# Kernel optimization log

Measured on AMD Instinct MI355X. Metric: run time of the kernel, lower is better.

The kernel has to match this reference:

```python
import jax, jax.numpy as jnp
import numpy as np

N = 16384      # total nodes (B graphs x 64 squares)
B = 256        # number of graphs
NODES = 64     # nodes per graph (chess board)
E = 131072     # directed edges (avg degree 8)
F_IN = 128
H = 256
GH = 4         # GAT heads
TH = 8         # transformer heads
L_GNN = 8
L_TF = 6
EPS = 1e-5


def layer_norm(x, g, b):
    m = jnp.mean(x, -1, keepdims=True)
    v = jnp.mean((x - m) ** 2, -1, keepdims=True)
    return (x - m) * jax.lax.rsqrt(v + EPS) * g + b


def setup_inputs() -> dict:
    key = jax.random.key(0)
    ks = iter(jax.random.split(key, 80))

    def nrm(shape, s=0.02):
        return jax.random.normal(next(ks), shape, jnp.float32) * s

    x = jax.random.normal(next(ks), (N, F_IN), jnp.float32)
    gid = jax.random.randint(next(ks), (E,), 0, B)
    off = jax.random.randint(next(ks), (2, E), 0, NODES)
    edge_index = gid[None, :] * NODES + off          # edges stay within a graph
    batch = jnp.arange(N, dtype=jnp.int32) // NODES
    piece_types = jax.random.randint(next(ks), (N,), 1, 7)
    return dict(
        x=x, edge_index=edge_index, batch=batch, piece_types=piece_types,
        emb_w=nrm((H, F_IN)), emb_b=nrm((H,)),
        gat_w=nrm((L_GNN, GH * H, H)), gat_as=nrm((L_GNN, GH, H)),
        gat_ad=nrm((L_GNN, GH, H)), gat_b=nrm((L_GNN, H)),
        gnn_g=jnp.ones((L_GNN, H)), gnn_beta=jnp.zeros((L_GNN, H)),
        ln1_g=jnp.ones((L_TF, H)), ln1_b=jnp.zeros((L_TF, H)),
        in_w=nrm((L_TF, 3 * H, H)), in_b=nrm((L_TF, 3 * H)),
        out_w=nrm((L_TF, H, H)), out_b=nrm((L_TF, H)),
        ln2_g=jnp.ones((L_TF, H)), ln2_b=jnp.zeros((L_TF, H)),
        ff1_w=nrm((L_TF, 4 * H, H)), ff1_b=nrm((L_TF, 4 * H)),
        ff2_w=nrm((L_TF, H, 4 * H)), ff2_b=nrm((L_TF, H)),
        pool_w=nrm((H,)), pool_b=nrm((1,)),
        vw1=nrm((H, H)), vb1=nrm((H,)), vw2=nrm((1, H)), vb2=nrm((1,)),
        pw1=nrm((H, H)), pb1=nrm((H,)), pw2=nrm((H, H)), pb2=nrm((H,)),
        uw1=nrm((H // 2, H)), ub1=nrm((H // 2,)), uw2=nrm((1, H // 2)), ub2=nrm((1,)))


def _forward(x, edge_index, batch, emb_w, emb_b, gat_w, gat_as, gat_ad, gat_b,
             gnn_g, gnn_beta, ln1_g, ln1_b, in_w, in_b, out_w, out_b, ln2_g,
             ln2_b, ff1_w, ff1_b, ff2_w, ff2_b, pool_w, pool_b, vw1, vb1, vw2,
             vb2, pw1, pb1, pw2, pb2, uw1, ub1, uw2, ub2):
    loops = jnp.arange(N, dtype=edge_index.dtype)     # GATConv add_self_loops=True
    src = jnp.concatenate([edge_index[0], loops])
    dst = jnp.concatenate([edge_index[1], loops])
    h = x @ emb_w.T + emb_b                           # [N,H] node embedding

    def gnn_layer(h, p):                              # ResidualGNNLayer
        W, a_s, a_d, bias, g, beta = p
        hp = (h @ W.T).reshape(N, GH, H)              # per-head projection
        al_s = jnp.sum(hp * a_s, -1)                  # [N,GH]
        al_d = jnp.sum(hp * a_d, -1)
        e = jax.nn.leaky_relu(al_s[src] + al_d[dst], 0.2)
        m = jax.ops.segment_max(e, dst, num_segments=N)
        ex = jnp.exp(e - m[dst])                      # segment softmax over dst
        den = jax.ops.segment_sum(ex, dst, num_segments=N)
        alpha = ex / den[dst]
        out = jax.ops.segment_sum(hp[src] * alpha[:, :, None], dst, num_segments=N)
        out = out.mean(1) + bias                      # concat=False -> head mean
        out = jax.nn.gelu(layer_norm(out, g, beta), approximate=False)
        return h + out, None                          # project = Identity

    h, _ = jax.lax.scan(gnn_layer, h, (gat_w, gat_as, gat_ad, gat_b, gnn_g, gnn_beta))

    # nn.MultiheadAttention defaults batch_first=False: axis0 (=B graphs) is the
    # sequence axis, axis1 (=64 nodes) is the batch axis — faithful to the source.
    xt = h.reshape(B, NODES, H)
    HD = H // TH

    def tf_layer(t, p):
        g1, b1, iw, ib, ow, ob, g2, b2, w1, fb1, w2, fb2 = p
        tn = layer_norm(t, g1, b1)
        q, k, v = jnp.split(tn @ iw.T + ib, 3, axis=-1)
        q = q.reshape(B, NODES, TH, HD)
        k = k.reshape(B, NODES, TH, HD)
        v = v.reshape(B, NODES, TH, HD)
        att = jnp.einsum('sbhd,tbhd->bhst', q, k) * (1.0 / HD ** 0.5)
        att = jax.nn.softmax(att, -1)
        o = jnp.einsum('bhst,tbhd->sbhd', att, v).reshape(B, NODES, H)
        t = t + (o @ ow.T + ob)
        tn = layer_norm(t, g2, b2)
        ff = jax.nn.gelu(tn @ w1.T + fb1, approximate=False) @ w2.T + fb2
        return t + ff, None

    xt, _ = jax.lax.scan(tf_layer, xt, (ln1_g, ln1_b, in_w, in_b, out_w, out_b,
                                        ln2_g, ln2_b, ff1_w, ff1_b, ff2_w, ff2_b))
    h = xt.reshape(N, H)

    # global attention pooling: softmax over ALL nodes (dim=0, as in the source)
    aw = jax.nn.softmax(h @ pool_w + pool_b[0], axis=0)
    g_rep = jax.ops.segment_sum(h * aw[:, None], batch, num_segments=B)
    value = jnp.tanh(jax.nn.gelu(g_rep @ vw1.T + vb1, approximate=False) @ vw2.T + vb2)[:, 0]
    policy = jax.nn.gelu(h @ pw1.T + pb1, approximate=False) @ pw2.T + pb2
    unc = jax.nn.softplus(jax.nn.gelu(g_rep @ uw1.T + ub1, approximate=False) @ uw2.T + ub2)[:, 0]
    return value, policy, unc


def reference(x, edge_index, batch, piece_types, emb_w, emb_b, gat_w, gat_as,
              gat_ad, gat_b, gnn_g, gnn_beta, ln1_g, ln1_b, in_w, in_b, out_w,
              out_b, ln2_g, ln2_b, ff1_w, ff1_b, ff2_w, ff2_b, pool_w, pool_b,
              vw1, vb1, vw2, vb2, pw1, pb1, pw2, pb2, uw1, ub1, uw2, ub2):
    # piece_types feeds PositionSpecificFeatureExtractor whose output is dead
    # code in the source forward (never used), so it is omitted here.
    return _forward(x, edge_index, batch, emb_w, emb_b, gat_w, gat_as, gat_ad,
                    gat_b, gnn_g, gnn_beta, ln1_g, ln1_b, in_w, in_b, out_w,
                    out_b, ln2_g, ln2_b, ff1_w, ff1_b, ff2_w, ff2_b, pool_w,
                    pool_b, vw1, vb1, vw2, vb2, pw1, pb1, pw2, pb2, uw1, ub1,
                    uw2, ub2)
```

## Files before the change

### kernel.cpp

```cpp
#include <hip/hip_runtime.h>
#include <hip/hip_bf16.h>

typedef __hip_bfloat16 bf16;
typedef __bf16 bf16x8 __attribute__((ext_vector_type(8)));
typedef float  f32x4  __attribute__((ext_vector_type(4)));

#define N_NODES 16384
#define HDIM    256
#define NE      131072
#define NE2     147456

__device__ __forceinline__ float b2f(bf16 v){ return __bfloat162float(v); }
__device__ __forceinline__ bf16  f2b(float v){ return __float2bfloat16(v); }
__device__ __forceinline__ float us2f(unsigned short u){
  union { unsigned int i; float f; } c; c.i = ((unsigned int)u) << 16; return c.f;
}
__device__ __forceinline__ unsigned short f2us(float f){
  bf16 h = __float2bfloat16(f);
  unsigned short u; __builtin_memcpy(&u, &h, 2); return u;
}
__device__ __forceinline__ float gelu_f(float x){
  return 0.5f * x * (1.0f + erff(x * 0.7071067811865476f));
}
__device__ __forceinline__ float wave_sum(float v){
  #pragma unroll
  for (int o = 32; o > 0; o >>= 1) v += __shfl_xor(v, o);
  return v;
}
__device__ __forceinline__ float wave_max(float v){
  #pragma unroll
  for (int o = 32; o > 0; o >>= 1) v = fmaxf(v, __shfl_xor(v, o));
  return v;
}

__device__ __forceinline__ float4 load4(const float* p){ return *(const float4*)p; }
__device__ __forceinline__ float4 load4(const bf16* p){
  ushort4 u = *(const ushort4*)p;
  return make_float4(us2f(u.x), us2f(u.y), us2f(u.z), us2f(u.w));
}
__device__ __forceinline__ void store4(float* p, float4 v){ *(float4*)p = v; }
__device__ __forceinline__ void store4(bf16* p, float4 v){
  ushort4 u = make_ushort4(f2us(v.x), f2us(v.y), f2us(v.z), f2us(v.w));
  *(ushort4*)p = u;
}
__device__ __forceinline__ void storev(float* p, float4 v){ *(float4*)p = v; }
__device__ __forceinline__ void storev(bf16*  p, float4 v){ store4(p, v); }

__device__ __forceinline__ void async_ld16(const bf16* g, unsigned short* l){
  __builtin_amdgcn_global_load_lds(
      (const __attribute__((address_space(1))) void*)g,
      (__attribute__((address_space(3))) void*)l, 16, 0, 0);
}

__global__ void detect_dtype(const unsigned short* __restrict__ x, int n, int* __restrict__ flags){
  int i = blockIdx.x * 256 + threadIdx.x;
  if (i < n) {
    unsigned short u = x[i];
    if ((u & 0x7F80) == 0x7F80) atomicOr(&flags[1], 1);
  }
}
struct ConvArgs {
  const void* src[35];
  unsigned short* dst[35];
  int cumg[36];
  int n[35];
};
__global__ void conv_all4(ConvArgs a, const int* __restrict__ flags){
  int gi = blockIdx.x * 256 + threadIdx.x;
  if (gi >= a.cumg[35]) return;
  int lo = 0, hi = 34;
  while (lo < hi) { int mid = (lo + hi + 1) >> 1; if (gi >= a.cumg[mid]) lo = mid; else hi = mid - 1; }
  int e0 = (gi - a.cumg[lo]) << 2;
  int n = a.n[lo];
  unsigned short* d = a.dst[lo];
  if (flags[1]) {
    const float* s = (const float*)a.src[lo];
    if (e0 + 4 <= n) {
      float4 v = *(const float4*)(s + e0);
      *(ushort4*)(d + e0) = make_ushort4(f2us(v.x), f2us(v.y), f2us(v.z), f2us(v.w));
    } else {
      for (int t = 0; t < n - e0; ++t) d[e0 + t] = f2us(s[e0 + t]);
    }
  } else {
    const unsigned short* s = (const unsigned short*)a.src[lo];
    if (e0 + 4 <= n) *(ushort4*)(d + e0) = *(const ushort4*)(s + e0);
    else for (int t = 0; t < n - e0; ++t) d[e0 + t] = s[e0 + t];
  }
}
__global__ void emit_out(const unsigned short* __restrict__ stage, void* __restrict__ out,
                         int n, const int* __restrict__ flags){
  int i = blockIdx.x * 256 + threadIdx.x;
  if (i >= n) return;
  if (flags[1]) ((float*)out)[i] = us2f(stage[i]);
  else          ((unsigned short*)out)[i] = stage[i];
}
__global__ void write_sentinel(bf16* out, float v){ out[threadIdx.x] = f2b(v); }

#define GF_GELU 1
#define GF_RES  2
#define GF_MIR  4
#define GF_ALS  8

template<typename TO, int FLAGS>
__global__ __launch_bounds__(256) void gemm2(
    const bf16* __restrict__ A, const bf16* __restrict__ W,
    const bf16* __restrict__ bias, const float* __restrict__ res,
    TO* __restrict__ C, bf16* __restrict__ C2, int M, int Nn, int K,
    const bf16* __restrict__ asp, const bf16* __restrict__ adp,
    float* __restrict__ alsp)
{
  __shared__ __align__(16) char ldsraw[36864];
  unsigned short* sA = (unsigned short*)ldsraw;
  unsigned short* sB = sA + 128 * 64;
  const int tid = threadIdx.x;
  const int wave = tid >> 6, lane = tid & 63;
  const int quad = lane >> 4, l16 = lane & 15;
  const int wm = wave & 1, wn = wave >> 1;
  const int row0 = blockIdx.y << 7, col0 = blockIdx.x << 7;
  const int lr = lane >> 3, lc = lane & 7;

  f32x4 acc[4][4] = {};

  for (int kt = 0; kt < K; kt += 64) {
    #pragma unroll
    for (int it = 0; it < 4; ++it) {
      int r0 = (wave << 5) + (it << 3);
      int rr = r0 + lr;
      int gch = lc ^ (rr & 7);
      async_ld16(A + (size_t)(row0 + rr) * K + kt + (gch << 3), sA + (r0 << 6));
      async_ld16(W + (size_t)(col0 + rr) * K + kt + (gch << 3), sB + (r0 << 6));
    }
    __syncthreads();
    #pragma unroll
    for (int kk = 0; kk < 2; ++kk) {
      bf16x8 af[4];
      #pragma unroll
      for (int i = 0; i < 4; ++i) {
        int m = (wm << 6) + (i << 4) + l16;
        af[i] = *(const bf16x8*)&sA[(m << 6) + ((((kk << 2) + quad) ^ (l16 & 7)) << 3)];
      }
      #pragma unroll
      for (int j = 0; j < 4; ++j) {
        int n = (wn << 6) + (j << 4) + l16;
        bf16x8 bfr = *(const bf16x8*)&sB[(n << 6) + ((((kk << 2) + quad) ^ (l16 & 7)) << 3)];
        #pragma unroll
        for (int i = 0; i < 4; ++i)
          acc[i][j] = __builtin_amdgcn_mfma_f32_16x16x32_bf16(af[i], bfr, acc[i][j], 0, 0, 0);
      }
    }
    __syncthreads();
  }

  float* ct = (float*)ldsraw + wave * (64 * 36);
  #pragma unroll
  for (int p = 0; p < 2; ++p) {
    #pragma unroll
    for (int i = 0; i < 4; ++i)
      #pragma unroll
      for (int r = 0; r < 4; ++r) {
        int row = (i << 4) + (quad << 2) + r;
        ct[row * 36 + l16]      = acc[i][(p << 1) + 0][r];
        ct[row * 36 + 16 + l16] = acc[i][(p << 1) + 1][r];
      }
    float4 sS = make_float4(0.f, 0.f, 0.f, 0.f);
    float4 sD = make_float4(0.f, 0.f, 0.f, 0.f);
    #pragma unroll
    for (int it2 = 0; it2 < 8; ++it2) {
      int row = (it2 << 3) + lr;
      int c4 = lc << 2;
      float4 v = *(const float4*)&ct[row * 36 + c4];
      int gcol = col0 + (wn << 6) + (p << 5) + c4;
      size_t gidx = (size_t)(row0 + (wm << 6) + row) * Nn + gcol;
      if (FLAGS & GF_ALS) {
        float asv = b2f(asp[row0 + (wm << 6) + row]);
        float adv = b2f(adp[row0 + (wm << 6) + row]);
        sS.x += asv * v.x; sS.y += asv * v.y; sS.z += asv * v.z; sS.w += asv * v.w;
        sD.x += adv * v.x; sD.y += adv * v.y; sD.z += adv * v.z; sD.w += adv * v.w;
      }
      if (bias) {
        float4 bv = load4(bias + gcol);
        v.x += bv.x; v.y += bv.y; v.z += bv.z; v.w += bv.w;
      }
      if (FLAGS & GF_GELU) {
        v.x = gelu_f(v.x); v.y = gelu_f(v.y); v.z = gelu_f(v.z); v.w = gelu_f(v.w);
      }
      if (FLAGS & GF_RES) {
        float4 rv = *(const float4*)&res[gidx];
        v.x += rv.x; v.y += rv.y; v.z += rv.z; v.w += rv.w;
      }
      storev(C + gidx, v);
      if (FLAGS & GF_MIR) store4(C2 + gidx, v);
    }
    if (FLAGS & GF_ALS) {
      #pragma unroll
      for (int o = 8; o < 64; o <<= 1) {
        sS.x += __shfl_xor(sS.x, o); sS.y += __shfl_xor(sS.y, o);
        sS.z += __shfl_xor(sS.z, o); sS.w += __shfl_xor(sS.w, o);
        sD.x += __shfl_xor(sD.x, o); sD.y += __shfl_xor(sD.y, o);
        sD.z += __shfl_xor(sD.z, o); sD.w += __shfl_xor(sD.w, o);
      }
      if (lr == 0) {
        int node = col0 + (wn << 6) + (p << 5) + (lc << 2);
        int hd2 = blockIdx.y >> 1;
        int slice = ((blockIdx.y & 1) << 1) | wm;
        *(float4*)&alsp[(size_t)((slice << 3) + hd2) * Nn + node] = sS;
        *(float4*)&alsp[(size_t)((slice << 3) + 4 + hd2) * Nn + node] = sD;
      }
    }
  }
}

__global__ __launch_bounds__(256) void gemm_rln(
    const bf16* __restrict__ A, const bf16* __restrict__ W,
    const bf16* __restrict__ bias, float* __restrict__ h,
    bf16* __restrict__ tn, const bf16* __restrict__ lng,
    const bf16* __restrict__ lnb, int K)
{
  __shared__ __align__(16) char ldsraw[66560];
  unsigned short* sA = (unsigned short*)ldsraw;
  unsigned short* sB = sA + 64 * 64;
  const int tid = threadIdx.x;
  const int wave = tid >> 6, lane = tid & 63;
  const int quad = lane >> 4, l16 = lane & 15;
  const int row0 = blockIdx.x << 6;
  const int lr = lane >> 3, lc = lane & 7;

  f32x4 acc[4][4] = {};

  for (int kt = 0; kt < K; kt += 64) {
    #pragma unroll
    for (int it = 0; it < 2; ++it) {
      int r0 = (wave << 4) + (it << 3);
      int rr = r0 + lr;
      int gch = lc ^ (rr & 7);
      async_ld16(A + (size_t)(row0 + rr) * K + kt + (gch << 3), sA + (r0 << 6));
    }
    #pragma unroll
    for (int it = 0; it < 8; ++it) {
      int r0 = (wave << 6) + (it << 3);
      int rr = r0 + lr;
      int gch = lc ^ (rr & 7);
      async_ld16(W + (size_t)rr * K + kt + (gch << 3), sB + (r0 << 6));
    }
    __syncthreads();
    #pragma unroll
    for (int kk = 0; kk < 2; ++kk) {
      bf16x8 af[4];
      #pragma unroll
      for (int i = 0; i < 4; ++i) {
        int m = (i << 4) + l16;
        af[i] = *(const bf16x8*)&sA[(m << 6) + ((((kk << 2) + quad) ^ (l16 & 7)) << 3)];
      }
      #pragma unroll
      for (int j = 0; j < 4; ++j) {
        int n = (wave << 6) + (j << 4) + l16;
        bf16x8 bfr = *(const bf16x8*)&sB[(n << 6) + ((((kk << 2) + quad) ^ (l16 & 7)) << 3)];
        #pragma unroll
        for (int i = 0; i < 4; ++i)
          acc[i][j] = __builtin_amdgcn_mfma_f32_16x16x32_bf16(af[i], bfr, acc[i][j], 0, 0, 0);
      }
    }
    __syncthreads();
  }

  float* ct = (float*)ldsraw;
  #pragma unroll
  for (int j = 0; j < 4; ++j) {
    int col = (wave << 6) + (j << 4) + l16;
    #pragma unroll
    for (int i = 0; i < 4; ++i)
      #pragma unroll
      for (int r = 0; r < 4; ++r)
        ct[((i << 4) + (quad << 2) + r) * 260 + col] = acc[i][j][r];
  }
  __syncthreads();

  const int row = tid >> 2, q = tid & 3;
  const int c0 = q << 6;
  size_t gr = (size_t)(row0 + row) * 256 + c0;
  float4 v[16];
  float s1 = 0.f;
  #pragma unroll
  for (int k = 0; k < 16; ++k) {
    float4 cv = *(const float4*)&ct[row * 260 + c0 + (k << 2)];
    float4 bv = load4(bias + c0 + (k << 2));
    float4 rv = *(const float4*)&h[gr + (k << 2)];
    v[k].x = cv.x + bv.x + rv.x;
    v[k].y = cv.y + bv.y + rv.y;
    v[k].z = cv.z + bv.z + rv.z;
    v[k].w = cv.w + bv.w + rv.w;
    *(float4*)&h[gr + (k << 2)] = v[k];
    s1 += v[k].x + v[k].y + v[k].z + v[k].w;
  }
  s1 += __shfl_xor(s1, 1); s1 += __shfl_xor(s1, 2);
  float mean = s1 * (1.0f / 256.0f);
  float s2 = 0.f;
  #pragma unroll
  for (int k = 0; k < 16; ++k) {
    float dx = v[k].x - mean, dy = v[k].y - mean, dz = v[k].z - mean, dw = v[k].w - mean;
    s2 += dx * dx + dy * dy + dz * dz + dw * dw;
  }
  s2 += __shfl_xor(s2, 1); s2 += __shfl_xor(s2, 2);
  float rstd = rsqrtf(s2 * (1.0f / 256.0f) + 1e-5f);
  #pragma unroll
  for (int k = 0; k < 16; ++k) {
    float4 gv = load4(lng + c0 + (k << 2));
    float4 bv2 = load4(lnb + c0 + (k << 2));
    float4 y;
    y.x = (v[k].x - mean) * rstd * gv.x + bv2.x;
    y.y = (v[k].y - mean) * rstd * gv.y + bv2.y;
    y.z = (v[k].z - mean) * rstd * gv.z + bv2.z;
    y.w = (v[k].w - mean) * rstd * gv.w + bv2.w;
    store4(tn + gr + (k << 2), y);
  }
}

__global__ void csr_count(const int* __restrict__ edst, int* __restrict__ cnt){
  int e = blockIdx.x * 256 + threadIdx.x;
  if (e < NE2) {
    int d = (e < NE) ? edst[e] : (e - NE);
    atomicAdd(&cnt[d], 1);
  }
}
__global__ __launch_bounds__(1024) void csr_scan(const int* __restrict__ cnt, int* __restrict__ off){
  __shared__ int ls[1024];
  int t = threadIdx.x;
  int base = t * 16;
  int loc[16]; int s = 0;
  #pragma unroll
  for (int j = 0; j < 16; ++j) { loc[j] = s; s += cnt[base + j]; }
  ls[t] = s;
  __syncthreads();
  for (int o = 1; o < 1024; o <<= 1) {
    int v = (t >= o) ? ls[t - o] : 0;
    __syncthreads();
    ls[t] += v;
    __syncthreads();
  }
  int pre = (t == 0) ? 0 : ls[t - 1];
  #pragma unroll
  for (int j = 0; j < 16; ++j) off[base + j] = pre + loc[j];
  if (t == 1023) off[N_NODES] = ls[1023];
}
__global__ void csr_fill(const int* __restrict__ edst, const int* __restrict__ off,
                         int* __restrict__ fillc, int* __restrict__ list){
  int e = blockIdx.x * 256 + threadIdx.x;
  if (e < NE2) {
    int d = (e < NE) ? edst[e] : (e - NE);
    int p = atomicAdd(&fillc[d], 1);
    list[off[d] + p] = e;
  }
}

#define ALF_S 68

__device__ __forceinline__ bf16x8 pack8(const float* v, float scale){
  unsigned short u[8];
  #pragma unroll
  for (int t = 0; t < 8; ++t) u[t] = f2us(v[t] * scale);
  bf16x8 r; __builtin_memcpy(&r, u, 16); return r;
}

__global__ __launch_bounds__(256) void gat_graph2(
    const int* __restrict__ esrc, const bf16* __restrict__ hpT_g,
    const int* __restrict__ off, const int* __restrict__ list,
    const float* __restrict__ alsp,
    bf16* __restrict__ msg4, int g0, int hn)
{
  __shared__ unsigned short hpT[256 * 64];
  __shared__ float alpha[64 * ALF_S];
  __shared__ float als[64], ald[64], dinv[64];

  const int hd = blockIdx.x & 3;
  const int lg = blockIdx.x >> 2;
  const int g  = g0 + lg;
  const int tid = threadIdx.x;
  const int wave = tid >> 6, lane = tid & 63;
  const int quad = lane >> 4, l16 = lane & 15;
  const int nd = tid >> 2;
  const int k4 = tid & 3;

  {
    const int rl = lane >> 3, jj = lane & 7;
    #pragma unroll
    for (int it = 0; it < 8; ++it) {
      int c = (it << 5) + (wave << 3) + rl;
      async_ld16(hpT_g + (size_t)((hd << 8) + c) * 16384 + (g << 6) + ((jj ^ (c & 7)) << 3),
                 hpT + (((it << 5) + (wave << 3)) << 6));
    }
  }
  if (tid < 128) {
    int n2 = tid & 63;
    int sd = (tid >> 6) << 2;
    float v = 0.f;
    #pragma unroll
    for (int sl = 0; sl < 4; ++sl)
      v += alsp[(size_t)((sl << 3) + sd + hd) * 16384 + (g << 6) + n2];
    if (sd) ald[n2] = v; else als[n2] = v;
  }
  #pragma unroll
  for (int idx = tid; idx < 64 * ALF_S; idx += 256) alpha[idx] = 0.f;
  __syncthreads();

  {
    int st = off[(g << 6) + nd];
    int deg = off[(g << 6) + nd + 1] - st;
    float ad = ald[nd];
    float mx = -1e30f;
    for (int e = k4; e < deg; e += 4) {
      int ed = list[st + e];
      int sl = ((ed < NE) ? esrc[ed] : (ed - NE)) - (g << 6);
      float v = als[sl] + ad;
      v = (v > 0.f) ? v : 0.2f * v;
      mx = fmaxf(mx, v);
    }
    mx = fmaxf(mx, __shfl_xor(mx, 1)); mx = fmaxf(mx, __shfl_xor(mx, 2));
    float den = 0.f;
    for (int e = k4; e < deg; e += 4) {
      int ed = list[st + e];
      int sl = ((ed < NE) ? esrc[ed] : (ed - NE)) - (g << 6);
      float v = als[sl] + ad;
      v = (v > 0.f) ? v : 0.2f * v;
      float w = __expf(v - mx);
      den += w;
      atomicAdd(&alpha[nd * ALF_S + sl], w);
    }
    den += __shfl_xor(den, 1); den += __shfl_xor(den, 2);
    if (k4 == 0) dinv[nd] = 1.0f / den;
  }
  __syncthreads();

  f32x4 acc[4][4] = {};
  #pragma unroll
  for (int kk = 0; kk < 2; ++kk) {
    bf16x8 af[4];
    #pragma unroll
    for (int i = 0; i < 4; ++i) {
      int m = (i << 4) + l16;
      const float* ap = &alpha[m * ALF_S + (kk << 5) + (quad << 3)];
      float av[8];
      float4 a0 = *(const float4*)ap, a1 = *(const float4*)(ap + 4);
      av[0]=a0.x; av[1]=a0.y; av[2]=a0.z; av[3]=a0.w;
      av[4]=a1.x; av[5]=a1.y; av[6]=a1.z; av[7]=a1.w;
      af[i] = pack8(av, dinv[m]);
    }
    #pragma unroll
    for (int j = 0; j < 4; ++j) {
      int c2 = (wave << 6) + (j << 4) + l16;
      int chunk = (kk << 2) + quad;
      bf16x8 bfr = *(const bf16x8*)&hpT[(c2 << 6) + ((chunk ^ (c2 & 7)) << 3)];
      #pragma unroll
      for (int i = 0; i < 4; ++i)
        acc[i][j] = __builtin_amdgcn_mfma_f32_16x16x32_bf16(af[i], bfr, acc[i][j], 0, 0, 0);
    }
  }

  #pragma unroll
  for (int j = 0; j < 4; ++j) {
    int col = (wave << 6) + (j << 4) + l16;
    #pragma unroll
    for (int i = 0; i < 4; ++i) {
      int rbase = (i << 4) + (quad << 2);
      #pragma unroll
      for (int r = 0; r < 4; ++r)
        msg4[((size_t)hd * hn + (lg << 6) + rbase + r) * 256 + col] = f2b(acc[i][j][r]);
    }
  }
}

__global__ __launch_bounds__(256) void gat_epi(
    const bf16* __restrict__ msg4, int hn, int n0,
    const bf16* __restrict__ bias, const bf16* __restrict__ gg, const bf16* __restrict__ gb,
    float* __restrict__ h, bf16* __restrict__ hb,
    const bf16* __restrict__ lng, const bf16* __restrict__ lnb, bf16* __restrict__ tno)
{
  int nl = blockIdx.x * 4 + (threadIdx.x >> 6);
  int lane = threadIdx.x & 63;
  int c = lane * 4;
  float4 s = make_float4(0.f, 0.f, 0.f, 0.f);
  #pragma unroll
  for (int hd = 0; hd < 4; ++hd) {
    float4 m = load4(msg4 + ((size_t)hd * hn + nl) * 256 + c);
    s.x += m.x; s.y += m.y; s.z += m.z; s.w += m.w;
  }
  float4 bv = load4(bias + c);
  float ox = s.x * 0.25f + bv.x, oy = s.y * 0.25f + bv.y;
  float oz = s.z * 0.25f + bv.z, ow = s.w * 0.25f + bv.w;
  float mean = wave_sum(ox + oy + oz + ow) * (1.0f / 256.0f);
  float dx = ox - mean, dy = oy - mean, dz = oz - mean, dw = ow - mean;
  float var = wave_sum(dx*dx + dy*dy + dz*dz + dw*dw) * (1.0f / 256.0f);
  float r = rsqrtf(var + 1e-5f);
  float4 gv = load4(gg + c); float4 b2 = load4(gb + c);
  size_t base = ((size_t)(n0 + nl)) * 256 + c;
  float4 hv = load4(h + base);
  hv.x += gelu_f(dx * r * gv.x + b2.x);
  hv.y += gelu_f(dy * r * gv.y + b2.y);
  hv.z += gelu_f(dz * r * gv.z + b2.z);
  hv.w += gelu_f(dw * r * gv.w + b2.w);
  store4(h + base, hv);
  store4(hb + base, hv);
  if (lng) {
    float m2 = wave_sum(hv.x + hv.y + hv.z + hv.w) * (1.0f / 256.0f);
    float ex = hv.x - m2, ey = hv.y - m2, ez = hv.z - m2, ew = hv.w - m2;
    float v2 = wave_sum(ex*ex + ey*ey + ez*ez + ew*ew) * (1.0f / 256.0f);
    float r2 = rsqrtf(v2 + 1e-5f);
    float4 g2 = load4(lng + c); float4 bb = load4(lnb + c);
    store4(tno + base, make_float4(ex*r2*g2.x + bb.x, ey*r2*g2.y + bb.y,
                                   ez*r2*g2.z + bb.z, ew*r2*g2.w + bb.w));
  }
}

__global__ __launch_bounds__(256) void ln_kernel(
    const float* __restrict__ x, bf16* __restrict__ y,
    const bf16* __restrict__ g, const bf16* __restrict__ b)
{
  int row = blockIdx.x * 4 + (threadIdx.x >> 6);
  int lane = threadIdx.x & 63;
  int c = lane * 4;
  float4 v = load4(x + (size_t)row * 256 + c);
  float mean = wave_sum(v.x + v.y + v.z + v.w) * (1.0f / 256.0f);
  float dx = v.x - mean, dy = v.y - mean, dz = v.z - mean, dw = v.w - mean;
  float var = wave_sum(dx*dx + dy*dy + dz*dz + dw*dw) * (1.0f / 256.0f);
  float r = rsqrtf(var + 1e-5f);
  float4 gv = load4(g + c); float4 bv = load4(b + c);
  store4(y + (size_t)row * 256 + c,
         make_float4(dx*r*gv.x + bv.x, dy*r*gv.y + bv.y, dz*r*gv.z + bv.z, dw*r*gv.w + bv.w));
}

#define VT_LDS 268
#define P_LDS  72

__global__ __launch_bounds__(256) void attn_mfma(
    const bf16* __restrict__ qkv, bf16* __restrict__ obuf)
{
  const int b  = blockIdx.x & 63;
  const int hh = blockIdx.x >> 6;
  __shared__ unsigned short VTs[32 * VT_LDS];
  __shared__ unsigned short Ps[4][64 * P_LDS];
  const int tid  = threadIdx.x;
  const int wave = tid >> 6, lane = tid & 63;
  const int quad = lane >> 4, l16 = lane & 15;

  {
    const bf16* vb = qkv + (size_t)(tid * 64 + b) * 768 + 512 + hh * 32;
    unsigned short vv[32];
    *(uint4*)&vv[0]  = *(const uint4*)(vb);
    *(uint4*)&vv[8]  = *(const uint4*)(vb + 8);
    *(uint4*)&vv[16] = *(const uint4*)(vb + 16);
    *(uint4*)&vv[24] = *(const uint4*)(vb + 24);
    #pragma unroll
    for (int d = 0; d < 32; ++d) VTs[d * VT_LDS + tid] = vv[d];
  }
  bf16x8 qf[4];
  #pragma unroll
  for (int i = 0; i < 4; ++i) {
    int s = (wave << 6) + (i << 4) + l16;
    qf[i] = *(const bf16x8*)(qkv + (size_t)(s * 64 + b) * 768 + hh * 32 + (quad << 3));
  }
  __syncthreads();

  const float scale = 0.17677669529663687f;
  f32x4 oacc[4][2] = {};
  float lsum[4][4] = {};
  unsigned short* Pw = &Ps[wave][0];

  for (int nt = 0; nt < 4; ++nt) {
    bf16x8 kf[4];
    #pragma unroll
    for (int j = 0; j < 4; ++j) {
      int t = (nt << 6) + (j << 4) + l16;
      kf[j] = *(const bf16x8*)(qkv + (size_t)(t * 64 + b) * 768 + 256 + hh * 32 + (quad << 3));
    }
    f32x4 zero = {0.f, 0.f, 0.f, 0.f};
    f32x4 sx[4][4];
    #pragma unroll
    for (int i = 0; i < 4; ++i)
      #pragma unroll
      for (int j = 0; j < 4; ++j)
        sx[i][j] = __builtin_amdgcn_mfma_f32_16x16x32_bf16(qf[i], kf[j], zero, 0, 0, 0);
    #pragma unroll
    for (int i = 0; i < 4; ++i) {
      #pragma unroll
      for (int r = 0; r < 4; ++r) {
        float p[4]; float rs = 0.f;
        #pragma unroll
        for (int j = 0; j < 4; ++j) {
          float sc = fminf(fmaxf(sx[i][j][r] * scale, -60.f), 60.f);
          p[j] = __expf(sc);
          rs += p[j];
        }
        #pragma unroll
        for (int o = 1; o < 16; o <<= 1) rs += __shfl_xor(rs, o);
        lsum[i][r] += rs;
        int row = (i << 4) + (quad << 2) + r;
        #pragma unroll
        for (int j = 0; j < 4; ++j)
          Pw[row * P_LDS + (j << 4) + l16] = f2us(p[j]);
      }
    }
    #pragma unroll
    for (int kk = 0; kk < 2; ++kk) {
      bf16x8 vf[2];
      #pragma unroll
      for (int j2 = 0; j2 < 2; ++j2)
        vf[j2] = *(const bf16x8*)&VTs[((j2 << 4) + l16) * VT_LDS + (nt << 6) + (kk << 5) + (quad << 3)];
      #pragma unroll
      for (int i2 = 0; i2 < 4; ++i2) {
        bf16x8 pf = *(const bf16x8*)&Pw[((i2 << 4) + l16) * P_LDS + (kk << 5) + (quad << 3)];
        #pragma unroll
        for (int j2 = 0; j2 < 2; ++j2)
          oacc[i2][j2] = __builtin_amdgcn_mfma_f32_16x16x32_bf16(pf, vf[j2], oacc[i2][j2], 0, 0, 0);
      }
    }
  }
  #pragma unroll
  for (int i = 0; i < 4; ++i) {
    #pragma unroll
    for (int r = 0; r < 4; ++r) {
      int srow = (wave << 6) + (i << 4) + (quad << 2) + r;
      float inv = 1.0f / lsum[i][r];
      #pragma unroll
      for (int j2 = 0; j2 < 2; ++j2)
        obuf[(size_t)(srow * 64 + b) * 256 + hh * 32 + (j2 << 4) + l16] = f2b(oacc[i][j2][r] * inv);
    }
  }
}

__global__ __launch_bounds__(256) void pool_logit(
    const float* __restrict__ h, const bf16* __restrict__ pw, const bf16* __restrict__ pb,
    float* __restrict__ logits)
{
  int n = blockIdx.x * 4 + (threadIdx.x >> 6); int lane = threadIdx.x & 63;
  float4 hv = load4(h + (size_t)n * 256 + lane * 4);
  float4 wv = load4(pw + lane * 4);
  float acc = wave_sum(hv.x*wv.x + hv.y*wv.y + hv.z*wv.z + hv.w*wv.w);
  if (lane == 0) logits[n] = acc + b2f(pb[0]);
}
__global__ __launch_bounds__(1024) void pool_reduce(
    const float* __restrict__ logits, float* __restrict__ red)
{
  __shared__ float sm[16];
  int t = threadIdx.x;
  float m = -1e30f;
  for (int i = t; i < N_NODES; i += 1024) m = fmaxf(m, logits[i]);
  m = wave_max(m);
  if ((t & 63) == 0) sm[t >> 6] = m;
  __syncthreads();
  if (t == 0) { float mm = sm[0]; for (int i = 1; i < 16; ++i) mm = fmaxf(mm, sm[i]); sm[0] = mm; }
  __syncthreads();
  float gmax = sm[0];
  __syncthreads();
  float s = 0.f;
  for (int i = t; i < N_NODES; i += 1024) s += expf(logits[i] - gmax);
  s = wave_sum(s);
  if ((t & 63) == 0) sm[t >> 6] = s;
  __syncthreads();
  if (t == 0) { float ss = 0.f; for (int i = 0; i < 16; ++i) ss += sm[i]; red[0] = gmax; red[1] = 1.0f / ss; }
}
__global__ __launch_bounds__(256) void pool_grep(
    const float* __restrict__ h, const float* __restrict__ logits,
    const float* __restrict__ red, bf16* __restrict__ g_rep)
{
  __shared__ float w[64];
  int g = blockIdx.x; int tid = threadIdx.x;
  if (tid < 64) w[tid] = expf(logits[g * 64 + tid] - red[0]) * red[1];
  __syncthreads();
  float acc = 0.f;
  for (int nd = 0; nd < 64; ++nd) acc += h[((size_t)g * 64 + nd) * 256 + tid] * w[nd];
  g_rep[(size_t)g * 256 + tid] = f2b(acc);
}
__global__ __launch_bounds__(256) void head_value(
    const float* __restrict__ vt, const bf16* __restrict__ w2, const bf16* __restrict__ b2,
    bf16* __restrict__ out)
{
  int gidx = blockIdx.x * 4 + (threadIdx.x >> 6); int lane = threadIdx.x & 63;
  float acc = 0.f;
  #pragma unroll
  for (int j = 0; j < 4; ++j) { int c = j * 64 + lane; acc += vt[(size_t)gidx * 256 + c] * b2f(w2[c]); }
  acc = wave_sum(acc);
  if (lane == 0) out[gidx] = f2b(tanhf(acc + b2f(b2[0])));
}
__global__ __launch_bounds__(256) void head_unc(
    const float* __restrict__ ut, const bf16* __restrict__ w2, const bf16* __restrict__ b2,
    bf16* __restrict__ out)
{
  int gidx = blockIdx.x * 4 + (threadIdx.x >> 6); int lane = threadIdx.x & 63;
  float acc = 0.f;
  #pragma unroll
  for (int j = 0; j < 2; ++j) { int c = j * 64 + lane; acc += ut[(size_t)gidx * 128 + c] * b2f(w2[c]); }
  acc = wave_sum(acc);
  if (lane == 0) {
    float x = acc + b2f(b2[0]);
    float sp = (x > 20.f) ? x : log1pf(expf(x));
    out[gidx] = f2b(sp);
  }
}

extern "C" void kernel_launch(void* const* d_in, const int* in_sizes, int n_in,
                              void* d_out, int out_size, void* d_ws, size_t ws_size,
                              hipStream_t stream)
{
  (void)out_size;
  const int* eidx = (const int*)d_in[1];

  char* ws = (char*)d_ws;
  size_t wo = 0;
  auto alloc = [&](size_t bytes) -> char* {
    char* p = ws + wo; wo += (bytes + 255) & ~(size_t)255; return p;
  };
  int*   flags = (int*)alloc(256);
  int*   cnt   = (int*)alloc((size_t)N_NODES * 4);
  int*   fillc = (int*)alloc((size_t)N_NODES * 4);
  size_t zero_end = wo;

  bf16* conv[38] = {};
  static const int fidx[35] = {0,4,5,6,7,8,9,10,11,12,13,14,15,16,17,18,19,
                               20,21,22,23,24,25,26,27,28,29,30,31,32,33,34,35,36,37};
  for (int j = 0; j < 35; ++j) {
    int idx = fidx[j];
    conv[idx] = (bf16*)alloc((size_t)in_sizes[idx] * 2);
  }
  float* h     = (float*)alloc((size_t)N_NODES * 256 * 4);
  bf16*  hb    = (bf16*) alloc((size_t)N_NODES * 256 * 2);
  bf16*  big   = (bf16*) alloc((size_t)N_NODES * 1024 * 2);
  const int OUT_ELEMS = 256 + N_NODES * 256 + 256;
  bf16*  tn     = (bf16*)alloc((size_t)N_NODES * 256 * 2);
  bf16*  ostage = (bf16*)alloc((size_t)OUT_ELEMS * 2);
  int*   off   = (int*)alloc((size_t)(N_NODES + 1) * 4);
  int*   list  = (int*)alloc((size_t)NE2 * 4);
  float* logits= (float*)alloc((size_t)N_NODES * 4);
  float* redb  = (float*)alloc(256);
  bf16*  g_rep = (bf16*)alloc((size_t)256 * 256 * 2);
  float* val_t = (float*)alloc((size_t)256 * 256 * 4);
  float* unc_t = (float*)alloc((size_t)256 * 128 * 4);
  float* alsp  = (float*)alloc((size_t)32 * N_NODES * 4);
  size_t base_needed = wo;

  if (n_in != 38)                   { write_sentinel<<<1,256,0,stream>>>((bf16*)d_out, 4.f);  return; }
  if (in_sizes[0] != N_NODES * 128) { write_sentinel<<<1,256,0,stream>>>((bf16*)d_out, 8.f);  return; }
  if (in_sizes[1] != 2 * NE)        { write_sentinel<<<1,256,0,stream>>>((bf16*)d_out, 16.f); return; }
  if (ws_size < base_needed)        { write_sentinel<<<1,256,0,stream>>>((bf16*)d_out, 32.f); return; }

  size_t msg_bytes = (size_t)4 * N_NODES * 256 * 2;
  bf16* msg4; int halves;
  if (ws_size >= base_needed + msg_bytes + 256) {
    msg4 = (bf16*)alloc(msg_bytes); halves = 1;
  } else {
    msg4 = tn; halves = 2;
  }

  hipMemsetAsync(d_ws, 0, zero_end, stream);

  detect_dtype<<<256, 256, 0, stream>>>((const unsigned short*)d_in[0], 65536, flags);
  {
    ConvArgs ca;
    int cum = 0;
    for (int j = 0; j < 35; ++j) {
      int idx = fidx[j];
      ca.src[j] = d_in[idx];
      ca.dst[j] = (unsigned short*)conv[idx];
      ca.cumg[j] = cum;
      ca.n[j] = in_sizes[idx];
      cum += (in_sizes[idx] + 3) >> 2;
    }
    ca.cumg[35] = cum;
    conv_all4<<<(cum + 255) / 256, 256, 0, stream>>>(ca, flags);
  }
  const bf16 *xb = conv[0], *emb_w = conv[4], *emb_b = conv[5], *gat_w = conv[6],
             *gat_as = conv[7], *gat_ad = conv[8], *gat_b = conv[9], *gnn_g = conv[10],
             *gnn_beta = conv[11], *ln1_g = conv[12], *ln1_b = conv[13], *in_w = conv[14],
             *in_b = conv[15], *out_w = conv[16], *out_b = conv[17], *ln2_g = conv[18],
             *ln2_b = conv[19], *ff1_w = conv[20], *ff1_b = conv[21], *ff2_w = conv[22],
             *ff2_b = conv[23], *pool_w = conv[24], *pool_b = conv[25],
             *vw1 = conv[26], *vb1 = conv[27], *vw2 = conv[28], *vb2 = conv[29],
             *pw1 = conv[30], *pb1 = conv[31], *pw2 = conv[32], *pb2 = conv[33],
             *uw1 = conv[34], *ub1 = conv[35], *uw2 = conv[36], *ub2 = conv[37];

  bf16* qkv  = big;
  bf16* obuf = big + (size_t)N_NODES * 768;
  bf16* hpT_g = big;
  bf16* ffb  = big;
  bf16* o_val = ostage;
  bf16* o_pol = ostage + 256;
  bf16* o_unc = ostage + 256 + (size_t)N_NODES * 256;

  csr_count<<<(NE2 + 255) / 256, 256, 0, stream>>>(eidx + NE, cnt);
  csr_scan<<<1, 1024, 0, stream>>>(cnt, off);
  csr_fill<<<(NE2 + 255) / 256, 256, 0, stream>>>(eidx + NE, off, fillc, list);

  gemm2<float, GF_MIR><<<dim3(2, 128), 256, 0, stream>>>(
      xb, emb_w, emb_b, nullptr, h, hb, N_NODES, 256, 128,
      nullptr, nullptr, nullptr);

  const int gph = 256 / halves;
  const int hn  = N_NODES / halves;
  for (int l = 0; l < 8; ++l) {
    gemm2<bf16, GF_ALS><<<dim3(128, 8), 256, 0, stream>>>(
        gat_w + (size_t)l * 1024 * 256, hb, nullptr, nullptr, hpT_g, nullptr,
        1024, N_NODES, 256, gat_as + l * 1024, gat_ad + l * 1024, alsp);
    const bf16* lng = (l == 7 && halves == 1) ? ln1_g : nullptr;
    const bf16* lnb = (l == 7 && halves == 1) ? ln1_b : nullptr;
    for (int ph = 0; ph < halves; ++ph) {
      gat_graph2<<<gph * 4, 256, 0, stream>>>(eidx, hpT_g, off, list, alsp,
          msg4, ph * gph, hn);
      gat_epi<<<hn / 4, 256, 0, stream>>>(msg4, hn, ph * hn,
          gat_b + l * 256, gnn_g + l * 256, gnn_beta + l * 256, h, hb,
          lng, lnb, tn);
    }
  }
  if (halves == 2)
    ln_kernel<<<N_NODES / 4, 256, 0, stream>>>(h, tn, ln1_g, ln1_b);

  for (int l = 0; l < 6; ++l) {
    gemm2<bf16, 0><<<dim3(6, 128), 256, 0, stream>>>(
        tn, in_w + (size_t)l * 768 * 256, in_b + l * 768, nullptr, qkv, nullptr, N_NODES, 768, 256,
        nullptr, nullptr, nullptr);
    attn_mfma<<<512, 256, 0, stream>>>(qkv, obuf);
    gemm_rln<<<N_NODES / 64, 256, 0, stream>>>(
        obuf, out_w + (size_t)l * 256 * 256, out_b + l * 256, h, tn,
        ln2_g + l * 256, ln2_b + l * 256, 256);
    gemm2<bf16, GF_GELU><<<dim3(8, 128), 256, 0, stream>>>(
        tn, ff1_w + (size_t)l * 1024 * 256, ff1_b + l * 1024, nullptr, ffb, nullptr, N_NODES, 1024, 256,
        nullptr, nullptr, nullptr);
    if (l < 5)
      gemm_rln<<<N_NODES / 64, 256, 0, stream>>>(
          ffb, ff2_w + (size_t)l * 256 * 1024, ff2_b + l * 256, h, tn,
          ln1_g + (l + 1) * 256, ln1_b + (l + 1) * 256, 1024);
    else
      gemm2<float, GF_RES | GF_MIR><<<dim3(2, 128), 256, 0, stream>>>(
          ffb, ff2_w + (size_t)l * 256 * 1024, ff2_b + l * 256, h, h, hb, N_NODES, 256, 1024,
          nullptr, nullptr, nullptr);
  }

  pool_logit<<<N_NODES / 4, 256, 0, stream>>>(h, pool_w, pool_b, logits);
  pool_reduce<<<1, 1024, 0, stream>>>(logits, redb);
  pool_grep<<<256, 256, 0, stream>>>(h, logits, redb, g_rep);
  gemm2<float, GF_GELU><<<dim3(2, 2), 256, 0, stream>>>(
      g_rep, vw1, vb1, nullptr, val_t, nullptr, 256, 256, 256,
      nullptr, nullptr, nullptr);
  head_value<<<64, 256, 0, stream>>>(val_t, vw2, vb2, o_val);
  gemm2<float, GF_GELU><<<dim3(1, 2), 256, 0, stream>>>(
      g_rep, uw1, ub1, nullptr, unc_t, nullptr, 256, 128, 256,
      nullptr, nullptr, nullptr);
  head_unc<<<64, 256, 0, stream>>>(unc_t, uw2, ub2, o_unc);
  gemm2<bf16, GF_GELU><<<dim3(2, 128), 256, 0, stream>>>(
      hb, pw1, pb1, nullptr, tn, nullptr, N_NODES, 256, 256,
      nullptr, nullptr, nullptr);
  gemm2<bf16, 0><<<dim3(2, 128), 256, 0, stream>>>(
      tn, pw2, pb2, nullptr, o_pol, nullptr, N_NODES, 256, 256,
      nullptr, nullptr, nullptr);

  emit_out<<<(OUT_ELEMS + 255) / 256, 256, 0, stream>>>(
      (const unsigned short*)ostage, d_out, OUT_ELEMS, flags);
}
```

Measured before the change: 1.550 ms.

## Fuse GAT head aggregation and epilogue into one per-graph kernel

Replaces the per-(graph, head) aggregation kernel and the separate bias/LayerNorm/GELU epilogue with one kernel per graph. It loops over the four heads, accumulating in registers, and double-buffers the next head's features into LDS with async loads. This removes the bf16 message buffer round-trip through global memory and a launch per layer. The cost is that the grid shrinks from 1024 blocks to 256, and each block uses about 85 KB of LDS, which lowers occupancy and parallelism.

Measured after the change: 1.861 ms. 20.0% more time.

```diff
diff --git a/kernel.cpp b/kernel.cpp
--- a/kernel.cpp
+++ b/kernel.cpp
@@ -361,170 +361,190 @@
   bf16x8 r; __builtin_memcpy(&r, u, 16); return r;
 }
 
-__global__ __launch_bounds__(256) void gat_graph2(
+__global__ __launch_bounds__(256) void gat_fused(
     const int* __restrict__ esrc, const bf16* __restrict__ hpT_g,
     const int* __restrict__ off, const int* __restrict__ list,
     const float* __restrict__ alsp,
-    bf16* __restrict__ msg4, int g0, int hn)
-{
-  __shared__ unsigned short hpT[256 * 64];
-  __shared__ float alpha[64 * ALF_S];
-  __shared__ float als[64], ald[64], dinv[64];
-
-  const int hd = blockIdx.x & 3;
-  const int lg = blockIdx.x >> 2;
-  const int g  = g0 + lg;
+    const bf16* __restrict__ bias, const bf16* __restrict__ gg, const bf16* __restrict__ gb,
+    float* __restrict__ h, bf16* __restrict__ hb,
+    const bf16* __restrict__ lng, const bf16* __restrict__ lnb, bf16* __restrict__ tno)
+{
+  __shared__ __align__(16) char lds[85504];
+  unsigned short* bufs = (unsigned short*)lds;
+  float* alpha = (float*)(lds + 65536);
+  float* alsS  = (float*)(lds + 82944);
+  float* alsD  = (float*)(lds + 83968);
+  float* dinv  = (float*)(lds + 84992);
+
+  const int g   = blockIdx.x;
   const int tid = threadIdx.x;
   const int wave = tid >> 6, lane = tid & 63;
   const int quad = lane >> 4, l16 = lane & 15;
-  const int nd = tid >> 2;
-  const int k4 = tid & 3;
-
+  const int nd = tid >> 2, k4 = tid & 3;
+  const int rl = lane >> 3, jj = lane & 7;
+
+  #pragma unroll
+  for (int it = 0; it < 8; ++it) {
+    int c = (it << 5) + (wave << 3) + rl;
+    async_ld16(hpT_g + (size_t)c * 16384 + (g << 6) + ((jj ^ (c & 7)) << 3),
+               bufs + (((it << 5) + (wave << 3)) << 6));
+  }
   {
-    const int rl = lane >> 3, jj = lane & 7;
-    #pragma unroll
-    for (int it = 0; it < 8; ++it) {
-      int c = (it << 5) + (wave << 3) + rl;
-      async_ld16(hpT_g + (size_t)((hd << 8) + c) * 16384 + (g << 6) + ((jj ^ (c & 7)) << 3),
-                 hpT + (((it << 5) + (wave << 3)) << 6));
-    }
-  }
-  if (tid < 128) {
-    int n2 = tid & 63;
-    int sd = (tid >> 6) << 2;
-    float v = 0.f;
-    #pragma unroll
-    for (int sl = 0; sl < 4; ++sl)
-      v += alsp[(size_t)((sl << 3) + sd + hd) * 16384 + (g << 6) + n2];
-    if (sd) ald[n2] = v; else als[n2] = v;
-  }
-  #pragma unroll
-  for (int idx = tid; idx < 64 * ALF_S; idx += 256) alpha[idx] = 0.f;
-  __syncthreads();
-
-  {
-    int st = off[(g << 6) + nd];
-    int deg = off[(g << 6) + nd + 1] - st;
-    float ad = ald[nd];
-    float mx = -1e30f;
-    for (int e = k4; e < deg; e += 4) {
-      int ed = list[st + e];
-      int sl = ((ed < NE) ? esrc[ed] : (ed - NE)) - (g << 6);
-      float v = als[sl] + ad;
-      v = (v > 0.f) ? v : 0.2f * v;
-      mx = fmaxf(mx, v);
-    }
-    mx = fmaxf(mx, __shfl_xor(mx, 1)); mx = fmaxf(mx, __shfl_xor(mx, 2));
-    float den = 0.f;
-    for (int e = k4; e < deg; e += 4) {
-      int ed = list[st + e];
-      int sl = ((ed < NE) ? esrc[ed] : (ed - NE)) - (g << 6);
-      float v = als[sl] + ad;
-      v = (v > 0.f) ? v : 0.2f * v;
-      float w = __expf(v - mx);
-      den += w;
-      atomicAdd(&alpha[nd * ALF_S + sl], w);
-    }
-    den += __shfl_xor(den, 1); den += __shfl_xor(den, 2);
-    if (k4 == 0) dinv[nd] = 1.0f / den;
-  }
-  __syncthreads();
+    int hd2 = tid >> 6, n2 = tid & 63;
+    float vs = 0.f, vd = 0.f;
+    #pragma unroll
+    for (int sl = 0; sl < 4; ++sl) {
+      vs += alsp[(size_t)((sl << 3) + hd2) * 16384 + (g << 6) + n2];
+      vd += alsp[(size_t)((sl << 3) + 4 + hd2) * 16384 + (g << 6) + n2];
+    }
+    alsS[(hd2 << 6) + n2] = vs;
+    alsD[(hd2 << 6) + n2] = vd;
+  }
+  const int st  = off[(g << 6) + nd];
+  const int deg = off[(g << 6) + nd + 1] - st;
 
   f32x4 acc[4][4] = {};
-  #pragma unroll
-  for (int kk = 0; kk < 2; ++kk) {
-    bf16x8 af[4];
-    #pragma unroll
-    for (int i = 0; i < 4; ++i) {
-      int m = (i << 4) + l16;
-      const float* ap = &alpha[m * ALF_S + (kk << 5) + (quad << 3)];
-      float av[8];
-      float4 a0 = *(const float4*)ap, a1 = *(const float4*)(ap + 4);
-      av[0]=a0.x; av[1]=a0.y; av[2]=a0.z; av[3]=a0.w;
-      av[4]=a1.x; av[5]=a1.y; av[6]=a1.z; av[7]=a1.w;
-      af[i] = pack8(av, dinv[m]);
-    }
-    #pragma unroll
-    for (int j = 0; j < 4; ++j) {
-      int c2 = (wave << 6) + (j << 4) + l16;
-      int chunk = (kk << 2) + quad;
-      bf16x8 bfr = *(const bf16x8*)&hpT[(c2 << 6) + ((chunk ^ (c2 & 7)) << 3)];
-      #pragma unroll
-      for (int i = 0; i < 4; ++i)
-        acc[i][j] = __builtin_amdgcn_mfma_f32_16x16x32_bf16(af[i], bfr, acc[i][j], 0, 0, 0);
-    }
-  }
-
+
+  for (int hd = 0; hd < 4; ++hd) {
+    unsigned short* buf = bufs + ((hd & 1) << 14);
+    #pragma unroll
+    for (int idx = tid; idx < 64 * ALF_S; idx += 256) alpha[idx] = 0.f;
+    __syncthreads();
+    if (hd < 3) {
+      unsigned short* nbuf = bufs + (((hd + 1) & 1) << 14);
+      #pragma unroll
+      for (int it = 0; it < 8; ++it) {
+        int c = (it << 5) + (wave << 3) + rl;
+        async_ld16(hpT_g + (size_t)(((hd + 1) << 8) + c) * 16384 + (g << 6) + ((jj ^ (c & 7)) << 3),
+                   nbuf + (((it << 5) + (wave << 3)) << 6));
+      }
+    }
+    {
+      const float* aS = alsS + (hd << 6);
+      float ad = alsD[(hd << 6) + nd];
+      float mx = -1e30f;
+      for (int e = k4; e < deg; e += 4) {
+        int ed = list[st + e];
+        int sl = ((ed < NE) ? esrc[ed] : (ed - NE)) - (g << 6);
+        float v = aS[sl] + ad;
+        v = (v > 0.f) ? v : 0.2f * v;
+        mx = fmaxf(mx, v);
+      }
+      mx = fmaxf(mx, __shfl_xor(mx, 1)); mx = fmaxf(mx, __shfl_xor(mx, 2));
+      float den = 0.f;
+      for (int e = k4; e < deg; e += 4) {
+        int ed = list[st + e];
+        int sl = ((ed < NE) ? esrc[ed] : (ed - NE)) - (g << 6);
+        float v = aS[sl] + ad;
+        v = (v > 0.f) ? v : 0.2f * v;
+        float w = __expf(v - mx);
+        den += w;
+        atomicAdd(&alpha[nd * ALF_S + sl], w);
+      }
+      den += __shfl_xor(den, 1); den += __shfl_xor(den, 2);
+      if (k4 == 0) dinv[nd] = 1.0f / den;
+    }
+    __syncthreads();
+    #pragma unroll
+    for (int kk = 0; kk < 2; ++kk) {
+      bf16x8 af[4];
+      #pragma unroll
+      for (int i = 0; i < 4; ++i) {
+        int m = (i << 4) + l16;
+        const float* ap = &alpha[m * ALF_S + (kk << 5) + (quad << 3)];
+        float av[8];
+        float4 a0 = *(const float4*)ap, a1 = *(const float4*)(ap + 4);
+        av[0]=a0.x; av[1]=a0.y; av[2]=a0.z; av[3]=a0.w;
+        av[4]=a1.x; av[5]=a1.y; av[6]=a1.z; av[7]=a1.w;
+        af[i] = pack8(av, dinv[m]);
+      }
+      #pragma unroll
+      for (int j = 0; j < 4; ++j) {
+        int c2 = (wave << 6) + (j << 4) + l16;
+        int chunk = (kk << 2) + quad;
+        bf16x8 bfr = *(const bf16x8*)&buf[(c2 << 6) + ((chunk ^ (c2 & 7)) << 3)];
+        #pragma unroll
+        for (int i = 0; i < 4; ++i)
+          acc[i][j] = __builtin_amdgcn_mfma_f32_16x16x32_bf16(af[i], bfr, acc[i][j], 0, 0, 0);
+      }
+    }
+    __syncthreads();
+  }
+
+  float* ct = (float*)lds;
   #pragma unroll
   for (int j = 0; j < 4; ++j) {
     int col = (wave << 6) + (j << 4) + l16;
     #pragma unroll
-    for (int i = 0; i < 4; ++i) {
-      int rbase = (i << 4) + (quad << 2);
+    for (int i = 0; i < 4; ++i)
       #pragma unroll
       for (int r = 0; r < 4; ++r)
-        msg4[((size_t)hd * hn + (lg << 6) + rbase + r) * 256 + col] = f2b(acc[i][j][r]);
-    }
-  }
-}
-
-__global__ __launch_bounds__(256) void gat_epi(
-    const bf16* __restrict__ msg4, int hn, int n0,
-    const bf16* __restrict__ bias, const bf16* __restrict__ gg, const bf16* __restrict__ gb,
-    float* __restrict__ h, bf16* __restrict__ hb,
-    const bf16* __restrict__ lng, const bf16* __restrict__ lnb, bf16* __restrict__ tno)
-{
-  int nl = blockIdx.x * 4 + (threadIdx.x >> 6);
-  int lane = threadIdx.x & 63;
-  int c = lane * 4;
-  float4 s = make_float4(0.f, 0.f, 0.f, 0.f);
-  #pragma unroll
-  for (int hd = 0; hd < 4; ++hd) {
-    float4 m = load4(msg4 + ((size_t)hd * hn + nl) * 256 + c);
-    s.x += m.x; s.y += m.y; s.z += m.z; s.w += m.w;
-  }
-  float4 bv = load4(bias + c);
-  float ox = s.x * 0.25f + bv.x, oy = s.y * 0.25f + bv.y;
-  float oz = s.z * 0.25f + bv.z, ow = s.w * 0.25f + bv.w;
-  float mean = wave_sum(ox + oy + oz + ow) * (1.0f / 256.0f);
-  float dx = ox - mean, dy = oy - mean, dz = oz - mean, dw = ow - mean;
-  float var = wave_sum(dx*dx + dy*dy + dz*dz + dw*dw) * (1.0f / 256.0f);
-  float r = rsqrtf(var + 1e-5f);
-  float4 gv = load4(gg + c); float4 b2 = load4(gb + c);
-  size_t base = ((size_t)(n0 + nl)) * 256 + c;
-  float4 hv = load4(h + base);
-  hv.x += gelu_f(dx * r * gv.x + b2.x);
-  hv.y += gelu_f(dy * r * gv.y + b2.y);
-  hv.z += gelu_f(dz * r * gv.z + b2.z);
-  hv.w += gelu_f(dw * r * gv.w + b2.w);
-  store4(h + base, hv);
-  store4(hb + base, hv);
+        ct[((i << 4) + (quad << 2) + r) * 260 + col] = acc[i][j][r];
+  }
+  __syncthreads();
+
+  const int row = tid >> 2, q = tid & 3;
+  const int c0 = q << 6;
+  size_t base = ((size_t)((g << 6) + row)) * 256 + c0;
+  float4 v[16];
+  float s1 = 0.f;
+  #pragma unroll
+  for (int k = 0; k < 16; ++k) {
+    float4 cv = *(const float4*)&ct[row * 260 + c0 + (k << 2)];
+    float4 bv = load4(bias + c0 + (k << 2));
+    v[k].x = cv.x * 0.25f + bv.x;
+    v[k].y = cv.y * 0.25f + bv.y;
+    v[k].z = cv.z * 0.25f + bv.z;
+    v[k].w = cv.w * 0.25f + bv.w;
+    s1 += v[k].x + v[k].y + v[k].z + v[k].w;
+  }
+  s1 += __shfl_xor(s1, 1); s1 += __shfl_xor(s1, 2);
+  float mean = s1 * (1.0f / 256.0f);
+  float s2 = 0.f;
+  #pragma unroll
+  for (int k = 0; k < 16; ++k) {
+    float dx = v[k].x - mean, dy = v[k].y - mean, dz = v[k].z - mean, dw = v[k].w - mean;
+    s2 += dx * dx + dy * dy + dz * dz + dw * dw;
+  }
+  s2 += __shfl_xor(s2, 1); s2 += __shfl_xor(s2, 2);
+  float rstd = rsqrtf(s2 * (1.0f / 256.0f) + 1e-5f);
+  float s3 = 0.f;
+  #pragma unroll
+  for (int k = 0; k < 16; ++k) {
+    float4 gv = load4(gg + c0 + (k << 2));
+    float4 b2 = load4(gb + c0 + (k << 2));
+    float4 rv = *(const float4*)&h[base + (k << 2)];
+    v[k].x = rv.x + gelu_f((v[k].x - mean) * rstd * gv.x + b2.x);
+    v[k].y = rv.y + gelu_f((v[k].y - mean) * rstd * gv.y + b2.y);
+    v[k].z = rv.z + gelu_f((v[k].z - mean) * rstd * gv.z + b2.z);
+    v[k].w = rv.w + gelu_f((v[k].w - mean) * rstd * gv.w + b2.w);
+    *(float4*)&h[base + (k << 2)] = v[k];
+    store4(hb + base + (k << 2), v[k]);
+    s3 += v[k].x + v[k].y + v[k].z + v[k].w;
+  }
   if (lng) {
-    float m2 = wave_sum(hv.x + hv.y + hv.z + hv.w) * (1.0f / 256.0f);
-    float ex = hv.x - m2, ey = hv.y - m2, ez = hv.z - m2, ew = hv.w - m2;
-    float v2 = wave_sum(ex*ex + ey*ey + ez*ez + ew*ew) * (1.0f / 256.0f);
-    float r2 = rsqrtf(v2 + 1e-5f);
-    float4 g2 = load4(lng + c); float4 bb = load4(lnb + c);
-    store4(tno + base, make_float4(ex*r2*g2.x + bb.x, ey*r2*g2.y + bb.y,
-                                   ez*r2*g2.z + bb.z, ew*r2*g2.w + bb.w));
-  }
-}
-
-__global__ __launch_bounds__(256) void ln_kernel(
-    const float* __restrict__ x, bf16* __restrict__ y,
-    const bf16* __restrict__ g, const bf16* __restrict__ b)
-{
-  int row = blockIdx.x * 4 + (threadIdx.x >> 6);
-  int lane = threadIdx.x & 63;
-  int c = lane * 4;
-  float4 v = load4(x + (size_t)row * 256 + c);
-  float mean = wave_sum(v.x + v.y + v.z + v.w) * (1.0f / 256.0f);
-  float dx = v.x - mean, dy = v.y - mean, dz = v.z - mean, dw = v.w - mean;
-  float var = wave_sum(dx*dx + dy*dy + dz*dz + dw*dw) * (1.0f / 256.0f);
-  float r = rsqrtf(var + 1e-5f);
-  float4 gv = load4(g + c); float4 bv = load4(b + c);
-  store4(y + (size_t)row * 256 + c,
-         make_float4(dx*r*gv.x + bv.x, dy*r*gv.y + bv.y, dz*r*gv.z + bv.z, dw*r*gv.w + bv.w));
+    s3 += __shfl_xor(s3, 1); s3 += __shfl_xor(s3, 2);
+    float m2 = s3 * (1.0f / 256.0f);
+    float s4 = 0.f;
+    #pragma unroll
+    for (int k = 0; k < 16; ++k) {
+      float dx = v[k].x - m2, dy = v[k].y - m2, dz = v[k].z - m2, dw = v[k].w - m2;
+      s4 += dx * dx + dy * dy + dz * dz + dw * dw;
+    }
+    s4 += __shfl_xor(s4, 1); s4 += __shfl_xor(s4, 2);
+    float r2 = rsqrtf(s4 * (1.0f / 256.0f) + 1e-5f);
+    #pragma unroll
+    for (int k = 0; k < 16; ++k) {
+      float4 g2 = load4(lng + c0 + (k << 2));
+      float4 bb = load4(lnb + c0 + (k << 2));
+      float4 y;
+      y.x = (v[k].x - m2) * r2 * g2.x + bb.x;
+      y.y = (v[k].y - m2) * r2 * g2.y + bb.y;
+      y.z = (v[k].z - m2) * r2 * g2.z + bb.z;
+      y.w = (v[k].w - m2) * r2 * g2.w + bb.w;
+      store4(tno + base + (k << 2), y);
+    }
+  }
 }
 
 #define VT_LDS 268
@@ -741,14 +761,6 @@
   if (in_sizes[1] != 2 * NE)        { write_sentinel<<<1,256,0,stream>>>((bf16*)d_out, 16.f); return; }
   if (ws_size < base_needed)        { write_sentinel<<<1,256,0,stream>>>((bf16*)d_out, 32.f); return; }
 
-  size_t msg_bytes = (size_t)4 * N_NODES * 256 * 2;
-  bf16* msg4; int halves;
-  if (ws_size >= base_needed + msg_bytes + 256) {
-    msg4 = (bf16*)alloc(msg_bytes); halves = 1;
-  } else {
-    msg4 = tn; halves = 2;
-  }
-
   hipMemsetAsync(d_ws, 0, zero_end, stream);
 
   detect_dtype<<<256, 256, 0, stream>>>((const unsigned short*)d_in[0], 65536, flags);
@@ -792,24 +804,15 @@
       xb, emb_w, emb_b, nullptr, h, hb, N_NODES, 256, 128,
       nullptr, nullptr, nullptr);
 
-  const int gph = 256 / halves;
-  const int hn  = N_NODES / halves;
   for (int l = 0; l < 8; ++l) {
     gemm2<bf16, GF_ALS><<<dim3(128, 8), 256, 0, stream>>>(
         gat_w + (size_t)l * 1024 * 256, hb, nullptr, nullptr, hpT_g, nullptr,
         1024, N_NODES, 256, gat_as + l * 1024, gat_ad + l * 1024, alsp);
-    const bf16* lng = (l == 7 && halves == 1) ? ln1_g : nullptr;
-    const bf16* lnb = (l == 7 && halves == 1) ? ln1_b : nullptr;
-    for (int ph = 0; ph < halves; ++ph) {
-      gat_graph2<<<gph * 4, 256, 0, stream>>>(eidx, hpT_g, off, list, alsp,
-          msg4, ph * gph, hn);
-      gat_epi<<<hn / 4, 256, 0, stream>>>(msg4, hn, ph * hn,
-          gat_b + l * 256, gnn_g + l * 256, gnn_beta + l * 256, h, hb,
-          lng, lnb, tn);
-    }
-  }
-  if (halves == 2)
-    ln_kernel<<<N_NODES / 4, 256, 0, stream>>>(h, tn, ln1_g, ln1_b);
+    gat_fused<<<256, 256, 0, stream>>>(
+        eidx, hpT_g, off, list, alsp,
+        gat_b + l * 256, gnn_g + l * 256, gnn_beta + l * 256, h, hb,
+        (l == 7) ? ln1_g : nullptr, (l == 7) ? ln1_b : nullptr, tn);
+  }
 
   for (int l = 0; l < 6; ++l) {
     gemm2<bf16, 0><<<dim3(6, 128), 256, 0, stream>>>(
```
